# Performance work log

Measured on AMD Instinct MI355X. Metric: run time of the kernel, lower is better.

## Reference

```python
import jax, jax.numpy as jnp
import numpy as np

B, N, ENC = 64, 49, 2048
DEC, ATT, EMB, V, TP1 = 512, 512, 300, 10000, 31


def setup_inputs() -> dict:
    key = jax.random.key(0)
    ks = jax.random.split(key, 20)
    s = 0.02
    inp = {
        "features": jax.random.normal(ks[0], (B, N, ENC), jnp.float32),
        "captions": jax.random.randint(ks[1], (B, TP1), 0, V, jnp.int64),
        "emb": jax.random.normal(ks[2], (V, EMB), jnp.float32) * s,
        "U_w": jax.random.normal(ks[3], (ATT, ENC), jnp.float32) * s,
        "U_b": jnp.zeros((ATT,), jnp.float32),
        "W_w": jax.random.normal(ks[4], (ATT, DEC), jnp.float32) * s,
        "W_b": jnp.zeros((ATT,), jnp.float32),
        "A_w": jax.random.normal(ks[5], (1, ATT), jnp.float32) * s,
        "A_b": jnp.zeros((1,), jnp.float32),
        "initH_w": jax.random.normal(ks[6], (DEC, ENC), jnp.float32) * s,
        "initH_b": jnp.zeros((DEC,), jnp.float32),
        "initC_w": jax.random.normal(ks[7], (DEC, ENC), jnp.float32) * s,
        "initC_b": jnp.zeros((DEC,), jnp.float32),
        "ih_w": jax.random.normal(ks[8], (4 * DEC, EMB + ENC), jnp.float32) * s,
        "ih_b": jnp.zeros((4 * DEC,), jnp.float32),
        "hh_w": jax.random.normal(ks[9], (4 * DEC, DEC), jnp.float32) * s,
        "hh_b": jnp.zeros((4 * DEC,), jnp.float32),
        "fcn_w": jax.random.normal(ks[10], (V, DEC), jnp.float32) * s,
        "fcn_b": jnp.zeros((V,), jnp.float32),
    }
    return inp


def reference(features, captions, emb, U_w, U_b, W_w, W_b, A_w, A_b,
              initH_w, initH_b, initC_w, initC_b,
              ih_w, ih_b, hh_w, hh_b, fcn_w, fcn_b):
    # embeds: [B, T+1, EMB]  (prembed lookup, frozen table)
    embeds = emb[captions]
    T = captions.shape[1] - 1  # static

    # init_hidden_state
    mean_f = features.mean(axis=1)                  # [B, ENC]
    h0 = mean_f @ initH_w.T + initH_b               # [B, DEC]
    c0 = mean_f @ initC_w.T + initC_b

    # U(features) is step-invariant: hoist out of the loop (same math)
    u_hs = jnp.einsum('bne,ae->bna', features, U_w) + U_b  # [B, N, ATT]

    xs = jnp.swapaxes(embeds[:, :T], 0, 1)          # [T, B, EMB]

    def step(carry, x):
        h, c = carry
        # additive attention
        w_ah = h @ W_w.T + W_b                       # [B, ATT]
        comb = jnp.tanh(u_hs + w_ah[:, None, :])     # [B, N, ATT]
        scores = jnp.einsum('bna,a->bn', comb, A_w[0]) + A_b[0]
        alpha = jax.nn.softmax(scores, axis=1)       # [B, N]
        context = jnp.einsum('bn,bne->be', alpha, features)  # [B, ENC]
        # LSTMCell
        lstm_in = jnp.concatenate([x, context], axis=1)
        gates = lstm_in @ ih_w.T + ih_b + h @ hh_w.T + hh_b
        i, f, g, o = jnp.split(gates, 4, axis=1)
        i, f, o = jax.nn.sigmoid(i), jax.nn.sigmoid(f), jax.nn.sigmoid(o)
        g = jnp.tanh(g)
        c = f * c + i * g
        h = o * jnp.tanh(c)
        # dropout in eval mode = identity
        out = h @ fcn_w.T + fcn_b                    # [B, V]
        return (h, c), (out, alpha)

    _, (preds, alphas) = jax.lax.scan(step, (h0, c0), xs)
    preds = jnp.swapaxes(preds, 0, 1)                # [B, T, V]
    alphas = jnp.swapaxes(alphas, 0, 1)              # [B, T, N]
    return preds, alphas
```

## Files before the change

### kernel.cpp

```cpp
#include <hip/hip_runtime.h>
#include <math.h>

#define B 64
#define NN 49
#define ENC 2048
#define DEC 512
#define ATT 512
#define EMB 300
#define VOC 10000
#define TT 30

typedef __attribute__((ext_vector_type(4))) float f32x4;
typedef __attribute__((ext_vector_type(4))) short s16x4;
typedef __attribute__((ext_vector_type(8))) short s16x8;
typedef unsigned short u16;

__device__ __forceinline__ float fast_tanh(float x) {
    float e = __expf(2.f * x);
    return 1.f - 2.f / (e + 1.f);
}
__device__ __forceinline__ float sigmoidf(float x) {
    return 1.f / (1.f + __expf(-x));
}
__device__ __forceinline__ u16 f2bf(float x) {
    unsigned u = __float_as_uint(x);
    unsigned r = u + 0x7FFFu + ((u >> 16) & 1u);
    return (u16)(r >> 16);
}
__device__ __forceinline__ float bf2f(u16 u) {
    return __uint_as_float((unsigned)u << 16);
}
__device__ __forceinline__ void split_bf16(float x, short& hi, short& lo) {
    u16 h = f2bf(x);
    float hf = __uint_as_float((unsigned)h << 16);
    hi = (short)h;
    lo = (short)f2bf(x - hf);
}
__device__ __forceinline__ s16x8 ld8(const short* p) {
    s16x4 a = *(const s16x4*)p;
    s16x4 b = *(const s16x4*)(p + 4);
    return __builtin_shufflevector(a, b, 0, 1, 2, 3, 4, 5, 6, 7);
}

__global__ __launch_bounds__(512) void mfma_nt(
    const float* __restrict__ A, int lda,
    const float* __restrict__ Bm, int ldb,
    const float* __restrict__ bias,
    float* __restrict__ C, int ldc,
    int M, int N, int K, int mode)
{
    __shared__ short Ah[128][40];
    __shared__ short Al[128][40];
    __shared__ short Bh[128][40];
    __shared__ short Bl[128][40];

    const int tid = threadIdx.x;
    const int m0 = blockIdx.y * 128, n0 = blockIdx.x * 128;
    const int wid = tid >> 6, lane = tid & 63;
    const int wm = wid >> 2, wn = wid & 3;
    const int lrow = lane & 15;
    const int lko = (lane >> 4) * 8;
    const int srow = tid >> 2;
    const int sk = (tid & 3) * 8;

    f32x4 acc[4][2];
    #pragma unroll
    for (int i = 0; i < 4; ++i)
        #pragma unroll
        for (int j = 0; j < 2; ++j)
            acc[i][j] = (f32x4){0.f, 0.f, 0.f, 0.f};

    const int nkt = (K + 31) >> 5;
    for (int kt = 0; kt < nkt; ++kt) {
        const int kb0 = kt * 32 + sk;
        {
            const int gr = m0 + srow;
            float v[8];
            if (gr < M && kb0 + 7 < K) {
                const float* p = A + (size_t)gr * lda + kb0;
                float4 x0 = *(const float4*)p;
                float4 x1 = *(const float4*)(p + 4);
                v[0] = x0.x; v[1] = x0.y; v[2] = x0.z; v[3] = x0.w;
                v[4] = x1.x; v[5] = x1.y; v[6] = x1.z; v[7] = x1.w;
            } else {
                #pragma unroll
                for (int j = 0; j < 8; ++j)
                    v[j] = (gr < M && kb0 + j < K) ? A[(size_t)gr * lda + kb0 + j] : 0.f;
            }
            s16x4 h0, h1, l0, l1;
            #pragma unroll
            for (int j = 0; j < 4; ++j) { short h, l; split_bf16(v[j], h, l); h0[j] = h; l0[j] = l; }
            #pragma unroll
            for (int j = 0; j < 4; ++j) { short h, l; split_bf16(v[4 + j], h, l); h1[j] = h; l1[j] = l; }
            *(s16x4*)&Ah[srow][sk] = h0; *(s16x4*)&Ah[srow][sk + 4] = h1;
            *(s16x4*)&Al[srow][sk] = l0; *(s16x4*)&Al[srow][sk + 4] = l1;
        }
        {
            const int gc = n0 + srow;
            float v[8];
            if (gc < N && kb0 + 7 < K) {
                const float* p = Bm + (size_t)gc * ldb + kb0;
                float4 x0 = *(const float4*)p;
                float4 x1 = *(const float4*)(p + 4);
                v[0] = x0.x; v[1] = x0.y; v[2] = x0.z; v[3] = x0.w;
                v[4] = x1.x; v[5] = x1.y; v[6] = x1.z; v[7] = x1.w;
            } else {
                #pragma unroll
                for (int j = 0; j < 8; ++j)
                    v[j] = (gc < N && kb0 + j < K) ? Bm[(size_t)gc * ldb + kb0 + j] : 0.f;
            }
            s16x4 h0, h1, l0, l1;
            #pragma unroll
            for (int j = 0; j < 4; ++j) { short h, l; split_bf16(v[j], h, l); h0[j] = h; l0[j] = l; }
            #pragma unroll
            for (int j = 0; j < 4; ++j) { short h, l; split_bf16(v[4 + j], h, l); h1[j] = h; l1[j] = l; }
            *(s16x4*)&Bh[srow][sk] = h0; *(s16x4*)&Bh[srow][sk + 4] = h1;
            *(s16x4*)&Bl[srow][sk] = l0; *(s16x4*)&Bl[srow][sk + 4] = l1;
        }
        __syncthreads();

        s16x8 bh[2], bl[2];
        #pragma unroll
        for (int nr = 0; nr < 2; ++nr) {
            const int col = wn * 32 + nr * 16 + lrow;
            bh[nr] = ld8(&Bh[col][lko]);
            bl[nr] = ld8(&Bl[col][lko]);
        }
        #pragma unroll
        for (int mr = 0; mr < 4; ++mr) {
            const int row = wm * 64 + mr * 16 + lrow;
            s16x8 ah = ld8(&Ah[row][lko]);
            s16x8 al = ld8(&Al[row][lko]);
            #pragma unroll
            for (int nr = 0; nr < 2; ++nr) {
                acc[mr][nr] = __builtin_amdgcn_mfma_f32_16x16x32_bf16(ah, bh[nr], acc[mr][nr], 0, 0, 0);
                acc[mr][nr] = __builtin_amdgcn_mfma_f32_16x16x32_bf16(ah, bl[nr], acc[mr][nr], 0, 0, 0);
                acc[mr][nr] = __builtin_amdgcn_mfma_f32_16x16x32_bf16(al, bh[nr], acc[mr][nr], 0, 0, 0);
            }
        }
        __syncthreads();
    }

    #pragma unroll
    for (int mr = 0; mr < 4; ++mr) {
        #pragma unroll
        for (int nr = 0; nr < 2; ++nr) {
            #pragma unroll
            for (int r = 0; r < 4; ++r) {
                const int row = m0 + wm * 64 + mr * 16 + (lane >> 4) * 4 + r;
                const int col = n0 + wn * 32 + nr * 16 + (lane & 15);
                if (row < M && col < N)
                    C[(size_t)row * ldc + col] = acc[mr][nr][r] + (bias ? bias[col] : 0.f);
            }
        }
    }
}

__global__ __launch_bounds__(512) void mfma_cat(
    const u16* __restrict__ fhi, const u16* __restrict__ flo,
    const float* __restrict__ U_w, const float* __restrict__ U_b,
    const float* __restrict__ ih_w,
    u16* __restrict__ uhs16, u16* __restrict__ fW16, int M)
{
    __shared__ short Ah[128][40];
    __shared__ short Al[128][40];
    __shared__ short Bh[128][40];
    __shared__ short Bl[128][40];

    const int tid = threadIdx.x;
    const int m0 = blockIdx.y * 128, n0 = blockIdx.x * 128;
    const int wid = tid >> 6, lane = tid & 63;
    const int wm = wid >> 2, wn = wid & 3;
    const int lrow = lane & 15;
    const int lko = (lane >> 4) * 8;
    const int srow = tid >> 2;
    const int sk = (tid & 3) * 8;

    const int gc = n0 + srow;
    const float* bp = (gc < 512) ? (U_w + (size_t)gc * 2048)
                                 : (ih_w + (size_t)(gc - 512) * 2348 + 300);
    const int gr = m0 + srow;
    const u16* ahp = fhi + (size_t)gr * 2048;
    const u16* alp = flo + (size_t)gr * 2048;

    f32x4 acc[4][2];
    #pragma unroll
    for (int i = 0; i < 4; ++i)
        #pragma unroll
        for (int j = 0; j < 2; ++j)
            acc[i][j] = (f32x4){0.f, 0.f, 0.f, 0.f};

    for (int kt = 0; kt < 64; ++kt) {
        const int kb0 = kt * 32 + sk;
        {
            s16x8 vh = {0,0,0,0,0,0,0,0}, vl = {0,0,0,0,0,0,0,0};
            if (gr < M) {
                vh = *(const s16x8*)(ahp + kb0);
                vl = *(const s16x8*)(alp + kb0);
            }
            *(s16x8*)&Ah[srow][sk] = vh;
            *(s16x8*)&Al[srow][sk] = vl;
        }
        {
            float4 x0 = *(const float4*)(bp + kb0);
            float4 x1 = *(const float4*)(bp + kb0 + 4);
            float v[8] = {x0.x, x0.y, x0.z, x0.w, x1.x, x1.y, x1.z, x1.w};
            s16x4 h0, h1, l0, l1;
            #pragma unroll
            for (int j = 0; j < 4; ++j) { short h, l; split_bf16(v[j], h, l); h0[j] = h; l0[j] = l; }
            #pragma unroll
            for (int j = 0; j < 4; ++j) { short h, l; split_bf16(v[4 + j], h, l); h1[j] = h; l1[j] = l; }
            *(s16x4*)&Bh[srow][sk] = h0; *(s16x4*)&Bh[srow][sk + 4] = h1;
            *(s16x4*)&Bl[srow][sk] = l0; *(s16x4*)&Bl[srow][sk + 4] = l1;
        }
        __syncthreads();

        s16x8 bh[2], bl[2];
        #pragma unroll
        for (int nr = 0; nr < 2; ++nr) {
            const int col = wn * 32 + nr * 16 + lrow;
            bh[nr] = ld8(&Bh[col][lko]);
            bl[nr] = ld8(&Bl[col][lko]);
        }
        #pragma unroll
        for (int mr = 0; mr < 4; ++mr) {
            const int row = wm * 64 + mr * 16 + lrow;
            s16x8 ah = ld8(&Ah[row][lko]);
            s16x8 al = ld8(&Al[row][lko]);
            #pragma unroll
            for (int nr = 0; nr < 2; ++nr) {
                acc[mr][nr] = __builtin_amdgcn_mfma_f32_16x16x32_bf16(ah, bh[nr], acc[mr][nr], 0, 0, 0);
                acc[mr][nr] = __builtin_amdgcn_mfma_f32_16x16x32_bf16(ah, bl[nr], acc[mr][nr], 0, 0, 0);
                acc[mr][nr] = __builtin_amdgcn_mfma_f32_16x16x32_bf16(al, bh[nr], acc[mr][nr], 0, 0, 0);
            }
        }
        __syncthreads();
    }

    #pragma unroll
    for (int mr = 0; mr < 4; ++mr) {
        #pragma unroll
        for (int nr = 0; nr < 2; ++nr) {
            #pragma unroll
            for (int r = 0; r < 4; ++r) {
                const int row = m0 + wm * 64 + mr * 16 + (lane >> 4) * 4 + r;
                const int col = n0 + wn * 32 + nr * 16 + (lane & 15);
                if (row < M) {
                    if (col < 512)
                        uhs16[(size_t)row * 512 + col] = f2bf(acc[mr][nr][r] + U_b[col]);
                    else
                        fW16[(size_t)row * 2048 + (col - 512)] = f2bf(acc[mr][nr][r]);
                }
            }
        }
    }
}

__global__ __launch_bounds__(512) void mfma_pre(
    const u16* __restrict__ Ahg, const u16* __restrict__ Alg,
    const u16* __restrict__ Bhg, const u16* __restrict__ Blg,
    const float* __restrict__ bias,
    float* __restrict__ C, int M, int N)
{
    __shared__ short Ah[128][40];
    __shared__ short Al[128][40];
    __shared__ short Bh[128][40];
    __shared__ short Bl[128][40];

    const int tid = threadIdx.x;
    const int m0 = blockIdx.y * 128, n0 = blockIdx.x * 128;
    const int wid = tid >> 6, lane = tid & 63;
    const int wm = wid >> 2, wn = wid & 3;
    const int lrow = lane & 15;
    const int lko = (lane >> 4) * 8;
    const int srow = tid >> 2;
    const int sk = (tid & 3) * 8;

    f32x4 acc[4][2];
    #pragma unroll
    for (int i = 0; i < 4; ++i)
        #pragma unroll
        for (int j = 0; j < 2; ++j)
            acc[i][j] = (f32x4){0.f, 0.f, 0.f, 0.f};

    for (int kt = 0; kt < 16; ++kt) {
        const int kb0 = kt * 32 + sk;
        {
            const int gr = m0 + srow;
            s16x8 vh = {0,0,0,0,0,0,0,0}, vl = {0,0,0,0,0,0,0,0};
            if (gr < M) {
                vh = *(const s16x8*)(Ahg + (size_t)gr * 512 + kb0);
                vl = *(const s16x8*)(Alg + (size_t)gr * 512 + kb0);
            }
            *(s16x8*)&Ah[srow][sk] = vh;
            *(s16x8*)&Al[srow][sk] = vl;
        }
        {
            const int gc = n0 + srow;
            s16x8 vh = {0,0,0,0,0,0,0,0}, vl = {0,0,0,0,0,0,0,0};
            if (gc < N) {
                vh = *(const s16x8*)(Bhg + (size_t)gc * 512 + kb0);
                vl = *(const s16x8*)(Blg + (size_t)gc * 512 + kb0);
            }
            *(s16x8*)&Bh[srow][sk] = vh;
            *(s16x8*)&Bl[srow][sk] = vl;
        }
        __syncthreads();

        s16x8 bh[2], bl[2];
        #pragma unroll
        for (int nr = 0; nr < 2; ++nr) {
            const int col = wn * 32 + nr * 16 + lrow;
            bh[nr] = ld8(&Bh[col][lko]);
            bl[nr] = ld8(&Bl[col][lko]);
        }
        #pragma unroll
        for (int mr = 0; mr < 4; ++mr) {
            const int row = wm * 64 + mr * 16 + lrow;
            s16x8 ah = ld8(&Ah[row][lko]);
            s16x8 al = ld8(&Al[row][lko]);
            #pragma unroll
            for (int nr = 0; nr < 2; ++nr) {
                acc[mr][nr] = __builtin_amdgcn_mfma_f32_16x16x32_bf16(ah, bh[nr], acc[mr][nr], 0, 0, 0);
                acc[mr][nr] = __builtin_amdgcn_mfma_f32_16x16x32_bf16(ah, bl[nr], acc[mr][nr], 0, 0, 0);
                acc[mr][nr] = __builtin_amdgcn_mfma_f32_16x16x32_bf16(al, bh[nr], acc[mr][nr], 0, 0, 0);
            }
        }
        __syncthreads();
    }

    #pragma unroll
    for (int mr = 0; mr < 4; ++mr) {
        #pragma unroll
        for (int nr = 0; nr < 2; ++nr) {
            #pragma unroll
            for (int r = 0; r < 4; ++r) {
                const int row = m0 + wm * 64 + mr * 16 + (lane >> 4) * 4 + r;
                const int col = n0 + wn * 32 + nr * 16 + (lane & 15);
                if (row < M && col < N) {
                    const float val = acc[mr][nr][r] + bias[col];
                    const int t = row >> 6, bb = row & 63;
                    C[(size_t)bb * (TT * VOC) + (size_t)t * VOC + col] = val;
                }
            }
        }
    }
}

__global__ __launch_bounds__(256) void k_mean(const float* __restrict__ f,
                                              float* __restrict__ mean_f)
{
    const int b = blockIdx.x;
    for (int e = threadIdx.x; e < ENC; e += 256) {
        float s = 0.f;
        for (int n = 0; n < NN; ++n) s += f[(size_t)(b * NN + n) * ENC + e];
        mean_f[(size_t)b * ENC + e] = s * (1.f / 49.f);
    }
}

__global__ __launch_bounds__(256) void k_init_partial(
    const float* __restrict__ mean_f,
    const float* __restrict__ iH_w, const float* __restrict__ iC_w,
    float* __restrict__ pbuf)
{
    const int tid = threadIdx.x;
    const int tx = tid & 15, ty = tid >> 4;
    const int n0 = blockIdx.x * 64;
    const int ks = blockIdx.y;
    __shared__ float As[16][64];
    __shared__ float Bs[16][64];
    float acc[4][4] = {};
    const int lrow = tid >> 2;
    const int lk = (tid & 3) * 4;
    for (int c = 0; c < 8; ++c) {
        const int kk = ks * 128 + c * 16 + lk;
        float4 av = *(const float4*)(mean_f + (size_t)lrow * 2048 + kk);
        const int col = n0 + lrow;
        const float* wp = (col < 512) ? (iH_w + (size_t)col * 2048)
                                      : (iC_w + (size_t)(col - 512) * 2048);
        float4 bv = *(const float4*)(wp + kk);
        As[lk + 0][lrow] = av.x; As[lk + 1][lrow] = av.y;
        As[lk + 2][lrow] = av.z; As[lk + 3][lrow] = av.w;
        Bs[lk + 0][lrow] = bv.x; Bs[lk + 1][lrow] = bv.y;
        Bs[lk + 2][lrow] = bv.z; Bs[lk + 3][lrow] = bv.w;
        __syncthreads();
        #pragma unroll
        for (int k = 0; k < 16; ++k) {
            float4 a = *(const float4*)&As[k][ty * 4];
            float4 b = *(const float4*)&Bs[k][tx * 4];
            acc[0][0] += a.x * b.x; acc[0][1] += a.x * b.y; acc[0][2] += a.x * b.z; acc[0][3] += a.x * b.w;
            acc[1][0] += a.y * b.x; acc[1][1] += a.y * b.y; acc[1][2] += a.y * b.z; acc[1][3] += a.y * b.w;
            acc[2][0] += a.z * b.x; acc[2][1] += a.z * b.y; acc[2][2] += a.z * b.z; acc[2][3] += a.z * b.w;
            acc[3][0] += a.w * b.x; acc[3][1] += a.w * b.y; acc[3][2] += a.w * b.z; acc[3][3] += a.w * b.w;
        }
        __syncthreads();
    }
    #pragma unroll
    for (int i = 0; i < 4; ++i) {
        const int r = ty * 4 + i;
        #pragma unroll
        for (int j = 0; j < 4; ++j)
            pbuf[(size_t)(ks * 64 + r) * 1024 + n0 + tx * 4 + j] = acc[i][j];
    }
}

__global__ __launch_bounds__(256) void k_init_reduce(
    const float* __restrict__ pbuf,
    const float* __restrict__ iH_b, const float* __restrict__ iC_b,
    float* __restrict__ h_cur, float* __restrict__ c_cur)
{
    const int idx = blockIdx.x * 256 + threadIdx.x;
    const int r = idx >> 10, c = idx & 1023;
    float s = 0.f;
    #pragma unroll
    for (int ks = 0; ks < 16; ++ks) s += pbuf[(size_t)(ks * 64 + r) * 1024 + c];
    if (c < 512) h_cur[r * 512 + c] = s + iH_b[c];
    else         c_cur[r * 512 + (c - 512)] = s + iC_b[c - 512];
}

__global__ __launch_bounds__(256) void k_embed(const int* __restrict__ cap,
                                               const float* __restrict__ emb,
                                               float* __restrict__ embeds)
{
    const int r = blockIdx.x;
    const int t = r >> 6, b = r & 63;
    const int c = cap[b * 31 + t];
    for (int j = threadIdx.x; j < EMB; j += 256)
        embeds[(size_t)r * EMB + j] = emb[(size_t)c * EMB + j];
}

__global__ void k_bias2(const float* __restrict__ a, const float* __restrict__ b,
                        float* __restrict__ o)
{
    const int j = blockIdx.x * 256 + threadIdx.x;
    if (j < 2048) o[j] = a[j] + b[j];
}

__global__ __launch_bounds__(256) void k_split(const float* __restrict__ src,
                                               u16* __restrict__ hi, u16* __restrict__ lo,
                                               int n)
{
    const int i = (blockIdx.x * 256 + threadIdx.x) * 4;
    if (i >= n) return;
    f32x4 v = *(const f32x4*)(src + i);
    s16x4 h4, l4;
    #pragma unroll
    for (int j = 0; j < 4; ++j) { short h, l; split_bf16(v[j], h, l); h4[j] = h; l4[j] = l; }
    *(s16x4*)(hi + i) = h4;
    *(s16x4*)(lo + i) = l4;
}

__global__ __launch_bounds__(256) void k_hw4(
    const float* __restrict__ h,
    const float* __restrict__ W_w, const float* __restrict__ W_b,
    const float* __restrict__ hh_w,
    float* __restrict__ wahp, float* __restrict__ ghhp)
{
    const int tid = threadIdx.x;
    const int tx = tid & 15, ty = tid >> 4;
    const int n0 = blockIdx.x * 64;
    const int ks = blockIdx.y;
    const float* Bp; const float* biasp; float* Cp; int c0, ldc;
    if (n0 < 512) { Bp = W_w + (size_t)n0 * 512; biasp = (ks == 0) ? W_b : nullptr; Cp = wahp + (size_t)ks * 32768; c0 = n0; ldc = 512; }
    else { Bp = hh_w + (size_t)(n0 - 512) * 512; biasp = nullptr; Cp = ghhp + (size_t)ks * 131072; c0 = n0 - 512; ldc = 2048; }

    __shared__ float As[64][68];
    __shared__ float Bs[64][68];
    float acc[4][4] = {};
    const int rt = tid >> 2;
    const int cs = (tid & 3) * 16;

    for (int kh = 0; kh < 2; ++kh) {
        const int kbase = ks * 128 + kh * 64;
        #pragma unroll
        for (int i = 0; i < 4; ++i) {
            const int c = cs + i * 4;
            *(f32x4*)&As[rt][c] = *(const f32x4*)(h + (size_t)rt * 512 + kbase + c);
            *(f32x4*)&Bs[rt][c] = *(const f32x4*)(Bp + (size_t)rt * 512 + kbase + c);
        }
        __syncthreads();
        #pragma unroll
        for (int k4 = 0; k4 < 16; ++k4) {
            f32x4 a0 = *(const f32x4*)&As[ty * 4 + 0][k4 * 4];
            f32x4 a1 = *(const f32x4*)&As[ty * 4 + 1][k4 * 4];
            f32x4 a2 = *(const f32x4*)&As[ty * 4 + 2][k4 * 4];
            f32x4 a3 = *(const f32x4*)&As[ty * 4 + 3][k4 * 4];
            f32x4 b0 = *(const f32x4*)&Bs[tx * 4 + 0][k4 * 4];
            f32x4 b1 = *(const f32x4*)&Bs[tx * 4 + 1][k4 * 4];
            f32x4 b2 = *(const f32x4*)&Bs[tx * 4 + 2][k4 * 4];
            f32x4 b3 = *(const f32x4*)&Bs[tx * 4 + 3][k4 * 4];
            #pragma unroll
            for (int e = 0; e < 4; ++e) {
                acc[0][0] += a0[e] * b0[e]; acc[0][1] += a0[e] * b1[e];
                acc[0][2] += a0[e] * b2[e]; acc[0][3] += a0[e] * b3[e];
                acc[1][0] += a1[e] * b0[e]; acc[1][1] += a1[e] * b1[e];
                acc[1][2] += a1[e] * b2[e]; acc[1][3] += a1[e] * b3[e];
                acc[2][0] += a2[e] * b0[e]; acc[2][1] += a2[e] * b1[e];
                acc[2][2] += a2[e] * b2[e]; acc[2][3] += a2[e] * b3[e];
                acc[3][0] += a3[e] * b0[e]; acc[3][1] += a3[e] * b1[e];
                acc[3][2] += a3[e] * b2[e]; acc[3][3] += a3[e] * b3[e];
            }
        }
        __syncthreads();
    }
    #pragma unroll
    for (int i = 0; i < 4; ++i) {
        const int r = ty * 4 + i;
        #pragma unroll
        for (int j = 0; j < 4; ++j) {
            const int cc = c0 + tx * 4 + j;
            Cp[(size_t)r * ldc + cc] = acc[i][j] + (biasp ? biasp[cc] : 0.f);
        }
    }
}

__global__ __launch_bounds__(512) void k_fused4(
    const u16* __restrict__ uhs16,
    const float* __restrict__ A_w, const float* __restrict__ A_b,
    const float* __restrict__ wahp,
    const float* __restrict__ ghhp,
    const float* __restrict__ pre_x,
    const u16* __restrict__ fW16,
    float* __restrict__ h_cur, float* __restrict__ c_cur,
    u16* __restrict__ Hall_h, u16* __restrict__ Hall_l,
    float* __restrict__ alphas, int s)
{
    const int bb = blockIdx.x;
    const int qq = blockIdx.y;
    const int tid = threadIdx.x;
    const int lane = tid & 63, w = tid >> 6;
    __shared__ float wah_l[512];
    __shared__ float red[64];
    __shared__ float al[64];
    __shared__ float ghl[512];
    __shared__ float gl[512];

    const int gate = tid >> 7, dloc = tid & 127;
    const int jcol = gate * 512 + qq * 128 + dloc;
    float ghv = pre_x[(size_t)(s * 64 + bb) * 2048 + jcol]
              + ghhp[(size_t)bb * 2048 + jcol]
              + ghhp[131072 + (size_t)bb * 2048 + jcol]
              + ghhp[262144 + (size_t)bb * 2048 + jcol]
              + ghhp[393216 + (size_t)bb * 2048 + jcol];
    float wv = wahp[bb * 512 + tid] + wahp[32768 + bb * 512 + tid]
             + wahp[65536 + bb * 512 + tid] + wahp[98304 + bb * 512 + tid];
    const float cload = c_cur[bb * 512 + qq * 128 + (tid & 127)];

    const int a0 = lane * 8;
    float aw8[8];
    #pragma unroll
    for (int k = 0; k < 8; ++k) aw8[k] = A_w[a0 + k];

    const int ngf = tid & 7, r = tid >> 3;
    const int gf = r >> 4, oc = r & 15;
    const int jb = gf * 512 + qq * 128 + oc * 8;
    const u16* fb = fW16 + (size_t)bb * NN * 2048 + jb;
    s16x8 pf[7];
    #pragma unroll
    for (int i = 0; i < 7; ++i) {
        const int n = ngf + 8 * i;
        if (n < NN) pf[i] = *(const s16x8*)(fb + (size_t)n * 2048);
        else        pf[i] = (s16x8){0, 0, 0, 0, 0, 0, 0, 0};
    }

    ghl[tid] = ghv;
    wah_l[tid] = wv;
    __syncthreads();

    float wh8[8];
    #pragma unroll
    for (int k = 0; k < 8; ++k) wh8[k] = wah_l[a0 + k];

    const u16* ub = uhs16 + (size_t)(bb * NN) * 512 + a0;
    #pragma unroll
    for (int i = 0; i < 7; ++i) {
        const int n = w + 8 * i;
        const int nc = (n < NN) ? n : 0;
        const s16x8 uv = *(const s16x8*)(ub + (size_t)nc * 512);
        float acc = 0.f;
        #pragma unroll
        for (int k = 0; k < 8; ++k)
            acc += aw8[k] * fast_tanh(bf2f((u16)uv[k]) + wh8[k]);
        #pragma unroll
        for (int m = 32; m; m >>= 1) acc += __shfl_xor(acc, m, 64);
        if (lane == 0 && n < NN) red[n] = acc + A_b[0];
    }
    __syncthreads();

    if (tid < 64) {
        const float sc = (tid < NN) ? red[tid] : -1e30f;
        float mx = sc;
        #pragma unroll
        for (int m = 32; m; m >>= 1) mx = fmaxf(mx, __shfl_xor(mx, m, 64));
        float e = (tid < NN) ? __expf(sc - mx) : 0.f;
        float sum = e;
        #pragma unroll
        for (int m = 32; m; m >>= 1) sum += __shfl_xor(sum, m, 64);
        const float av = e / sum;
        al[tid] = av;
        if (qq == 0 && tid < NN)
            alphas[(size_t)bb * (TT * NN) + (size_t)s * NN + tid] = av;
    }
    __syncthreads();

    float a8[8] = {0.f, 0.f, 0.f, 0.f, 0.f, 0.f, 0.f, 0.f};
    #pragma unroll
    for (int i = 0; i < 7; ++i) {
        const int n = ngf + 8 * i;
        const float av = al[n];
        #pragma unroll
        for (int k = 0; k < 8; ++k)
            a8[k] += av * bf2f((u16)pf[i][k]);
    }
    #pragma unroll
    for (int m = 1; m < 8; m <<= 1)
        #pragma unroll
        for (int k = 0; k < 8; ++k)
            a8[k] += __shfl_xor(a8[k], m, 64);
    if (ngf == 0) {
        const int base = gf * 128 + oc * 8;
        #pragma unroll
        for (int k = 0; k < 8; ++k)
            gl[base + k] = a8[k] + ghl[base + k];
    }
    __syncthreads();

    if (tid < 128) {
        const int dd = qq * 128 + tid;
        const float ig = sigmoidf(gl[tid]);
        const float fg = sigmoidf(gl[128 + tid]);
        const float gg = fast_tanh(gl[256 + tid]);
        const float og = sigmoidf(gl[384 + tid]);
        const float cv = fg * cload + ig * gg;
        const float hv = og * fast_tanh(cv);
        c_cur[bb * 512 + dd] = cv;
        h_cur[bb * 512 + dd] = hv;
        short hh, hl;
        split_bf16(hv, hh, hl);
        Hall_h[(size_t)(s * 64 + bb) * 512 + dd] = (u16)hh;
        Hall_l[(size_t)(s * 64 + bb) * 512 + dd] = (u16)hl;
    }
}

extern "C" void kernel_launch(void* const* d_in, const int* in_sizes, int n_in,
                              void* d_out, int out_size, void* d_ws, size_t ws_size,
                              hipStream_t stream)
{
    const float* features = (const float*)d_in[0];
    const int*   captions = (const int*)d_in[1];
    const float* emb      = (const float*)d_in[2];
    const float* U_w      = (const float*)d_in[3];
    const float* U_b      = (const float*)d_in[4];
    const float* W_w      = (const float*)d_in[5];
    const float* W_b      = (const float*)d_in[6];
    const float* A_w      = (const float*)d_in[7];
    const float* A_b      = (const float*)d_in[8];
    const float* iH_w     = (const float*)d_in[9];
    const float* iH_b     = (const float*)d_in[10];
    const float* iC_w     = (const float*)d_in[11];
    const float* iC_b     = (const float*)d_in[12];
    const float* ih_w     = (const float*)d_in[13];
    const float* ih_b     = (const float*)d_in[14];
    const float* hh_w     = (const float*)d_in[15];
    const float* hh_b     = (const float*)d_in[16];
    const float* fcn_w    = (const float*)d_in[17];
    const float* fcn_b    = (const float*)d_in[18];

    float* out    = (float*)d_out;
    float* alphas = out + (size_t)B * TT * VOC;

    float* ws     = (float*)d_ws;
    u16*  fW16    = (u16*)ws;
    u16*  uhs16   = (u16*)(ws + 3211264);
    float* pre_x  = ws + 4014080;
    u16*  Hall_h  = (u16*)(ws + 7946240);
    u16*  Hall_l  = (u16*)(ws + 8437760);
    float* mean_f = ws + 8929280;
    float* h_cur  = ws + 9060352;
    float* c_cur  = ws + 9093120;
    float* wahp   = ws + 9125888;
    float* ghhp   = ws + 9256960;
    float* embeds = ws + 9781248;
    float* bias2  = ws + 10357248;
    u16*  fhi     = (u16*)(ws + 10359296);
    u16*  flo     = (u16*)(ws + 13570560);
    float* pbuf   = ws;
    u16*  fcnw_h  = fhi;
    u16*  fcnw_l  = flo;

    k_mean<<<64, 256, 0, stream>>>(features, mean_f);
    k_init_partial<<<dim3(16, 16), 256, 0, stream>>>(mean_f, iH_w, iC_w, pbuf);
    k_init_reduce<<<256, 256, 0, stream>>>(pbuf, iH_b, iC_b, h_cur, c_cur);

    k_embed<<<1920, 256, 0, stream>>>(captions, emb, embeds);
    k_bias2<<<8, 256, 0, stream>>>(ih_b, hh_b, bias2);
    k_split<<<6272, 256, 0, stream>>>(features, fhi, flo, B * NN * ENC);
    mfma_cat<<<dim3(20, 25), 512, 0, stream>>>(fhi, flo, U_w, U_b, ih_w, uhs16, fW16, B * NN);
    mfma_nt<<<dim3(16, 15), 512, 0, stream>>>(embeds, EMB, ih_w, 2348, bias2, pre_x, 2048, TT * B, 2048, EMB, 0);

    k_hw4<<<dim3(40, 4), 256, 0, stream>>>(h_cur, W_w, W_b, hh_w, wahp, ghhp);
    for (int s = 0; s < TT; ++s) {
        k_fused4<<<dim3(64, 4), 512, 0, stream>>>(uhs16, A_w, A_b, wahp, ghhp, pre_x, fW16,
                                                  h_cur, c_cur, Hall_h, Hall_l, alphas, s);
        if (s < TT - 1)
            k_hw4<<<dim3(40, 4), 256, 0, stream>>>(h_cur, W_w, W_b, hh_w, wahp, ghhp);
    }

    k_split<<<5000, 256, 0, stream>>>(fcn_w, fcnw_h, fcnw_l, VOC * DEC);
    mfma_pre<<<dim3(79, 15), 512, 0, stream>>>(Hall_h, Hall_l, fcnw_h, fcnw_l, fcn_b,
                                               out, TT * B, VOC);
}
```

Before: 925.1 us.

## Pre-split ih_w, fuse embedding gather into GEMM, widen recurrent split-K

Result: no change. 928.6 us (+0.4%).

```diff
diff --git a/kernel.cpp b/kernel.cpp
--- a/kernel.cpp
+++ b/kernel.cpp
@@ -42,12 +42,11 @@
     return __builtin_shufflevector(a, b, 0, 1, 2, 3, 4, 5, 6, 7);
 }
 
-__global__ __launch_bounds__(512) void mfma_nt(
-    const float* __restrict__ A, int lda,
-    const float* __restrict__ Bm, int ldb,
-    const float* __restrict__ bias,
-    float* __restrict__ C, int ldc,
-    int M, int N, int K, int mode)
+__global__ __launch_bounds__(512) void mfma_cat2(
+    const u16* __restrict__ fhi, const u16* __restrict__ flo,
+    const float* __restrict__ U_w, const float* __restrict__ U_b,
+    const u16* __restrict__ ihw_h, const u16* __restrict__ ihw_l,
+    u16* __restrict__ uhs16, u16* __restrict__ fW16, int M)
 {
     __shared__ short Ah[128][40];
     __shared__ short Al[128][40];
@@ -63,122 +62,7 @@
     const int srow = tid >> 2;
     const int sk = (tid & 3) * 8;
 
-    f32x4 acc[4][2];
-    #pragma unroll
-    for (int i = 0; i < 4; ++i)
-        #pragma unroll
-        for (int j = 0; j < 2; ++j)
-            acc[i][j] = (f32x4){0.f, 0.f, 0.f, 0.f};
-
-    const int nkt = (K + 31) >> 5;
-    for (int kt = 0; kt < nkt; ++kt) {
-        const int kb0 = kt * 32 + sk;
-        {
-            const int gr = m0 + srow;
-            float v[8];
-            if (gr < M && kb0 + 7 < K) {
-                const float* p = A + (size_t)gr * lda + kb0;
-                float4 x0 = *(const float4*)p;
-                float4 x1 = *(const float4*)(p + 4);
-                v[0] = x0.x; v[1] = x0.y; v[2] = x0.z; v[3] = x0.w;
-                v[4] = x1.x; v[5] = x1.y; v[6] = x1.z; v[7] = x1.w;
-            } else {
-                #pragma unroll
-                for (int j = 0; j < 8; ++j)
-                    v[j] = (gr < M && kb0 + j < K) ? A[(size_t)gr * lda + kb0 + j] : 0.f;
-            }
-            s16x4 h0, h1, l0, l1;
-            #pragma unroll
-            for (int j = 0; j < 4; ++j) { short h, l; split_bf16(v[j], h, l); h0[j] = h; l0[j] = l; }
-            #pragma unroll
-            for (int j = 0; j < 4; ++j) { short h, l; split_bf16(v[4 + j], h, l); h1[j] = h; l1[j] = l; }
-            *(s16x4*)&Ah[srow][sk] = h0; *(s16x4*)&Ah[srow][sk + 4] = h1;
-            *(s16x4*)&Al[srow][sk] = l0; *(s16x4*)&Al[srow][sk + 4] = l1;
-        }
-        {
-            const int gc = n0 + srow;
-            float v[8];
-            if (gc < N && kb0 + 7 < K) {
-                const float* p = Bm + (size_t)gc * ldb + kb0;
-                float4 x0 = *(const float4*)p;
-                float4 x1 = *(const float4*)(p + 4);
-                v[0] = x0.x; v[1] = x0.y; v[2] = x0.z; v[3] = x0.w;
-                v[4] = x1.x; v[5] = x1.y; v[6] = x1.z; v[7] = x1.w;
-            } else {
-                #pragma unroll
-                for (int j = 0; j < 8; ++j)
-                    v[j] = (gc < N && kb0 + j < K) ? Bm[(size_t)gc * ldb + kb0 + j] : 0.f;
-            }
-            s16x4 h0, h1, l0, l1;
-            #pragma unroll
-            for (int j = 0; j < 4; ++j) { short h, l; split_bf16(v[j], h, l); h0[j] = h; l0[j] = l; }
-            #pragma unroll
-            for (int j = 0; j < 4; ++j) { short h, l; split_bf16(v[4 + j], h, l); h1[j] = h; l1[j] = l; }
-            *(s16x4*)&Bh[srow][sk] = h0; *(s16x4*)&Bh[srow][sk + 4] = h1;
-            *(s16x4*)&Bl[srow][sk] = l0; *(s16x4*)&Bl[srow][sk + 4] = l1;
-        }
-        __syncthreads();
-
-        s16x8 bh[2], bl[2];
-        #pragma unroll
-        for (int nr = 0; nr < 2; ++nr) {
-            const int col = wn * 32 + nr * 16 + lrow;
-            bh[nr] = ld8(&Bh[col][lko]);
-            bl[nr] = ld8(&Bl[col][lko]);
-        }
-        #pragma unroll
-        for (int mr = 0; mr < 4; ++mr) {
-            const int row = wm * 64 + mr * 16 + lrow;
-            s16x8 ah = ld8(&Ah[row][lko]);
-            s16x8 al = ld8(&Al[row][lko]);
-            #pragma unroll
-            for (int nr = 0; nr < 2; ++nr) {
-                acc[mr][nr] = __builtin_amdgcn_mfma_f32_16x16x32_bf16(ah, bh[nr], acc[mr][nr], 0, 0, 0);
-                acc[mr][nr] = __builtin_amdgcn_mfma_f32_16x16x32_bf16(ah, bl[nr], acc[mr][nr], 0, 0, 0);
-                acc[mr][nr] = __builtin_amdgcn_mfma_f32_16x16x32_bf16(al, bh[nr], acc[mr][nr], 0, 0, 0);
-            }
-        }
-        __syncthreads();
-    }
-
-    #pragma unroll
-    for (int mr = 0; mr < 4; ++mr) {
-        #pragma unroll
-        for (int nr = 0; nr < 2; ++nr) {
-            #pragma unroll
-            for (int r = 0; r < 4; ++r) {
-                const int row = m0 + wm * 64 + mr * 16 + (lane >> 4) * 4 + r;
-                const int col = n0 + wn * 32 + nr * 16 + (lane & 15);
-                if (row < M && col < N)
-                    C[(size_t)row * ldc + col] = acc[mr][nr][r] + (bias ? bias[col] : 0.f);
-            }
-        }
-    }
-}
-
-__global__ __launch_bounds__(512) void mfma_cat(
-    const u16* __restrict__ fhi, const u16* __restrict__ flo,
-    const float* __restrict__ U_w, const float* __restrict__ U_b,
-    const float* __restrict__ ih_w,
-    u16* __restrict__ uhs16, u16* __restrict__ fW16, int M)
-{
-    __shared__ short Ah[128][40];
-    __shared__ short Al[128][40];
-    __shared__ short Bh[128][40];
-    __shared__ short Bl[128][40];
-
-    const int tid = threadIdx.x;
-    const int m0 = blockIdx.y * 128, n0 = blockIdx.x * 128;
-    const int wid = tid >> 6, lane = tid & 63;
-    const int wm = wid >> 2, wn = wid & 3;
-    const int lrow = lane & 15;
-    const int lko = (lane >> 4) * 8;
-    const int srow = tid >> 2;
-    const int sk = (tid & 3) * 8;
-
     const int gc = n0 + srow;
-    const float* bp = (gc < 512) ? (U_w + (size_t)gc * 2048)
-                                 : (ih_w + (size_t)(gc - 512) * 2348 + 300);
     const int gr = m0 + srow;
     const u16* ahp = fhi + (size_t)gr * 2048;
     const u16* alp = flo + (size_t)gr * 2048;
@@ -201,7 +85,8 @@
             *(s16x8*)&Ah[srow][sk] = vh;
             *(s16x8*)&Al[srow][sk] = vl;
         }
-        {
+        if (n0 < 512) {
+            const float* bp = U_w + (size_t)gc * 2048;
             float4 x0 = *(const float4*)(bp + kb0);
             float4 x1 = *(const float4*)(bp + kb0 + 4);
             float v[8] = {x0.x, x0.y, x0.z, x0.w, x1.x, x1.y, x1.z, x1.w};
@@ -212,6 +97,9 @@
             for (int j = 0; j < 4; ++j) { short h, l; split_bf16(v[4 + j], h, l); h1[j] = h; l1[j] = l; }
             *(s16x4*)&Bh[srow][sk] = h0; *(s16x4*)&Bh[srow][sk + 4] = h1;
             *(s16x4*)&Bl[srow][sk] = l0; *(s16x4*)&Bl[srow][sk + 4] = l1;
+        } else {
+            *(s16x8*)&Bh[srow][sk] = *(const s16x8*)(ihw_h + (size_t)(gc - 512) * 2048 + kb0);
+            *(s16x8*)&Bl[srow][sk] = *(const s16x8*)(ihw_l + (size_t)(gc - 512) * 2048 + kb0);
         }
         __syncthreads();
 
@@ -251,6 +139,120 @@
                     else
                         fW16[(size_t)row * 2048 + (col - 512)] = f2bf(acc[mr][nr][r]);
                 }
+            }
+        }
+    }
+}
+
+__global__ __launch_bounds__(512) void mfma_prex(
+    const int* __restrict__ cap,
+    const float* __restrict__ emb,
+    const float* __restrict__ ih_w,
+    const float* __restrict__ bias2,
+    float* __restrict__ pre_x)
+{
+    __shared__ short Ah[128][40];
+    __shared__ short Al[128][40];
+    __shared__ short Bh[128][40];
+    __shared__ short Bl[128][40];
+
+    const int tid = threadIdx.x;
+    const int m0 = blockIdx.y * 128, n0 = blockIdx.x * 128;
+    const int wid = tid >> 6, lane = tid & 63;
+    const int wm = wid >> 2, wn = wid & 3;
+    const int lrow = lane & 15;
+    const int lko = (lane >> 4) * 8;
+    const int srow = tid >> 2;
+    const int sk = (tid & 3) * 8;
+
+    const int gr = m0 + srow;
+    const int tt = gr >> 6, bbs = gr & 63;
+    const float* ap = emb + (size_t)cap[bbs * 31 + tt] * 300;
+    const int gc = n0 + srow;
+    const float* bp = ih_w + (size_t)gc * 2348;
+
+    f32x4 acc[4][2];
+    #pragma unroll
+    for (int i = 0; i < 4; ++i)
+        #pragma unroll
+        for (int j = 0; j < 2; ++j)
+            acc[i][j] = (f32x4){0.f, 0.f, 0.f, 0.f};
+
+    for (int kt = 0; kt < 10; ++kt) {
+        const int kb0 = kt * 32 + sk;
+        {
+            float v[8];
+            if (kb0 + 7 < 300) {
+                float4 x0 = *(const float4*)(ap + kb0);
+                float4 x1 = *(const float4*)(ap + kb0 + 4);
+                v[0] = x0.x; v[1] = x0.y; v[2] = x0.z; v[3] = x0.w;
+                v[4] = x1.x; v[5] = x1.y; v[6] = x1.z; v[7] = x1.w;
+            } else {
+                #pragma unroll
+                for (int j = 0; j < 8; ++j)
+                    v[j] = (kb0 + j < 300) ? ap[kb0 + j] : 0.f;
+            }
+            s16x4 h0, h1, l0, l1;
+            #pragma unroll
+            for (int j = 0; j < 4; ++j) { short h, l; split_bf16(v[j], h, l); h0[j] = h; l0[j] = l; }
+            #pragma unroll
+            for (int j = 0; j < 4; ++j) { short h, l; split_bf16(v[4 + j], h, l); h1[j] = h; l1[j] = l; }
+            *(s16x4*)&Ah[srow][sk] = h0; *(s16x4*)&Ah[srow][sk + 4] = h1;
+            *(s16x4*)&Al[srow][sk] = l0; *(s16x4*)&Al[srow][sk + 4] = l1;
+        }
+        {
+            float v[8];
+            if (kb0 + 7 < 300) {
+                float4 x0 = *(const float4*)(bp + kb0);
+                float4 x1 = *(const float4*)(bp + kb0 + 4);
+                v[0] = x0.x; v[1] = x0.y; v[2] = x0.z; v[3] = x0.w;
+                v[4] = x1.x; v[5] = x1.y; v[6] = x1.z; v[7] = x1.w;
+            } else {
+                #pragma unroll
+                for (int j = 0; j < 8; ++j)
+                    v[j] = (kb0 + j < 300) ? bp[kb0 + j] : 0.f;
+            }
+            s16x4 h0, h1, l0, l1;
+            #pragma unroll
+            for (int j = 0; j < 4; ++j) { short h, l; split_bf16(v[j], h, l); h0[j] = h; l0[j] = l; }
+            #pragma unroll
+            for (int j = 0; j < 4; ++j) { short h, l; split_bf16(v[4 + j], h, l); h1[j] = h; l1[j] = l; }
+            *(s16x4*)&Bh[srow][sk] = h0; *(s16x4*)&Bh[srow][sk + 4] = h1;
+            *(s16x4*)&Bl[srow][sk] = l0; *(s16x4*)&Bl[srow][sk + 4] = l1;
+        }
+        __syncthreads();
+
+        s16x8 bh[2], bl[2];
+        #pragma unroll
+        for (int nr = 0; nr < 2; ++nr) {
+            const int col = wn * 32 + nr * 16 + lrow;
+            bh[nr] = ld8(&Bh[col][lko]);
+            bl[nr] = ld8(&Bl[col][lko]);
+        }
+        #pragma unroll
+        for (int mr = 0; mr < 4; ++mr) {
+            const int row = wm * 64 + mr * 16 + lrow;
+            s16x8 ah = ld8(&Ah[row][lko]);
+            s16x8 al = ld8(&Al[row][lko]);
+            #pragma unroll
+            for (int nr = 0; nr < 2; ++nr) {
+                acc[mr][nr] = __builtin_amdgcn_mfma_f32_16x16x32_bf16(ah, bh[nr], acc[mr][nr], 0, 0, 0);
+                acc[mr][nr] = __builtin_amdgcn_mfma_f32_16x16x32_bf16(ah, bl[nr], acc[mr][nr], 0, 0, 0);
+                acc[mr][nr] = __builtin_amdgcn_mfma_f32_16x16x32_bf16(al, bh[nr], acc[mr][nr], 0, 0, 0);
+            }
+        }
+        __syncthreads();
+    }
+
+    #pragma unroll
+    for (int mr = 0; mr < 4; ++mr) {
+        #pragma unroll
+        for (int nr = 0; nr < 2; ++nr) {
+            #pragma unroll
+            for (int r = 0; r < 4; ++r) {
+                const int row = m0 + wm * 64 + mr * 16 + (lane >> 4) * 4 + r;
+                const int col = n0 + wn * 32 + nr * 16 + (lane & 15);
+                pre_x[(size_t)row * 2048 + col] = acc[mr][nr][r] + bias2[col];
             }
         }
     }
@@ -418,17 +420,6 @@
     else         c_cur[r * 512 + (c - 512)] = s + iC_b[c - 512];
 }
 
-__global__ __launch_bounds__(256) void k_embed(const int* __restrict__ cap,
-                                               const float* __restrict__ emb,
-                                               float* __restrict__ embeds)
-{
-    const int r = blockIdx.x;
-    const int t = r >> 6, b = r & 63;
-    const int c = cap[b * 31 + t];
-    for (int j = threadIdx.x; j < EMB; j += 256)
-        embeds[(size_t)r * EMB + j] = emb[(size_t)c * EMB + j];
-}
-
 __global__ void k_bias2(const float* __restrict__ a, const float* __restrict__ b,
                         float* __restrict__ o)
 {
@@ -450,7 +441,26 @@
     *(s16x4*)(lo + i) = l4;
 }
 
-__global__ __launch_bounds__(256) void k_hw4(
+__global__ __launch_bounds__(256) void k_splitW(const float* __restrict__ ih_w,
+                                                u16* __restrict__ hi, u16* __restrict__ lo)
+{
+    const int r = blockIdx.x;
+    const float* src = ih_w + (size_t)r * 2348 + 300;
+    u16* hp = hi + (size_t)r * 2048;
+    u16* lp = lo + (size_t)r * 2048;
+    const int c = threadIdx.x * 8;
+    #pragma unroll
+    for (int g = 0; g < 2; ++g) {
+        f32x4 v = *(const f32x4*)(src + c + g * 4);
+        s16x4 h4, l4;
+        #pragma unroll
+        for (int j = 0; j < 4; ++j) { short h, l; split_bf16(v[j], h, l); h4[j] = h; l4[j] = l; }
+        *(s16x4*)(hp + c + g * 4) = h4;
+        *(s16x4*)(lp + c + g * 4) = l4;
+    }
+}
+
+__global__ __launch_bounds__(256) void k_hw8(
     const float* __restrict__ h,
     const float* __restrict__ W_w, const float* __restrict__ W_b,
     const float* __restrict__ hh_w,
@@ -469,52 +479,49 @@
     float acc[4][4] = {};
     const int rt = tid >> 2;
     const int cs = (tid & 3) * 16;
-
-    for (int kh = 0; kh < 2; ++kh) {
-        const int kbase = ks * 128 + kh * 64;
-        #pragma unroll
-        for (int i = 0; i < 4; ++i) {
-            const int c = cs + i * 4;
-            *(f32x4*)&As[rt][c] = *(const f32x4*)(h + (size_t)rt * 512 + kbase + c);
-            *(f32x4*)&Bs[rt][c] = *(const f32x4*)(Bp + (size_t)rt * 512 + kbase + c);
-        }
-        __syncthreads();
-        #pragma unroll
-        for (int k4 = 0; k4 < 16; ++k4) {
-            f32x4 a0 = *(const f32x4*)&As[ty * 4 + 0][k4 * 4];
-            f32x4 a1 = *(const f32x4*)&As[ty * 4 + 1][k4 * 4];
-            f32x4 a2 = *(const f32x4*)&As[ty * 4 + 2][k4 * 4];
-            f32x4 a3 = *(const f32x4*)&As[ty * 4 + 3][k4 * 4];
-            f32x4 b0 = *(const f32x4*)&Bs[tx * 4 + 0][k4 * 4];
-            f32x4 b1 = *(const f32x4*)&Bs[tx * 4 + 1][k4 * 4];
-            f32x4 b2 = *(const f32x4*)&Bs[tx * 4 + 2][k4 * 4];
-            f32x4 b3 = *(const f32x4*)&Bs[tx * 4 + 3][k4 * 4];
-            #pragma unroll
-            for (int e = 0; e < 4; ++e) {
-                acc[0][0] += a0[e] * b0[e]; acc[0][1] += a0[e] * b1[e];
-                acc[0][2] += a0[e] * b2[e]; acc[0][3] += a0[e] * b3[e];
-                acc[1][0] += a1[e] * b0[e]; acc[1][1] += a1[e] * b1[e];
-                acc[1][2] += a1[e] * b2[e]; acc[1][3] += a1[e] * b3[e];
-                acc[2][0] += a2[e] * b0[e]; acc[2][1] += a2[e] * b1[e];
-                acc[2][2] += a2[e] * b2[e]; acc[2][3] += a2[e] * b3[e];
-                acc[3][0] += a3[e] * b0[e]; acc[3][1] += a3[e] * b1[e];
-                acc[3][2] += a3[e] * b2[e]; acc[3][3] += a3[e] * b3[e];
-            }
-        }
-        __syncthreads();
-    }
+    const int kbase = ks * 64;
+
     #pragma unroll
     for (int i = 0; i < 4; ++i) {
-        const int r = ty * 4 + i;
+        const int c = cs + i * 4;
+        *(f32x4*)&As[rt][c] = *(const f32x4*)(h + (size_t)rt * 512 + kbase + c);
+        *(f32x4*)&Bs[rt][c] = *(const f32x4*)(Bp + (size_t)rt * 512 + kbase + c);
+    }
+    __syncthreads();
+    #pragma unroll 4
+    for (int k4 = 0; k4 < 16; ++k4) {
+        f32x4 a0 = *(const f32x4*)&As[ty + 0][k4 * 4];
+        f32x4 a1 = *(const f32x4*)&As[ty + 16][k4 * 4];
+        f32x4 a2 = *(const f32x4*)&As[ty + 32][k4 * 4];
+        f32x4 a3 = *(const f32x4*)&As[ty + 48][k4 * 4];
+        f32x4 b0 = *(const f32x4*)&Bs[tx + 0][k4 * 4];
+        f32x4 b1 = *(const f32x4*)&Bs[tx + 16][k4 * 4];
+        f32x4 b2 = *(const f32x4*)&Bs[tx + 32][k4 * 4];
+        f32x4 b3 = *(const f32x4*)&Bs[tx + 48][k4 * 4];
+        #pragma unroll
+        for (int e = 0; e < 4; ++e) {
+            acc[0][0] += a0[e] * b0[e]; acc[0][1] += a0[e] * b1[e];
+            acc[0][2] += a0[e] * b2[e]; acc[0][3] += a0[e] * b3[e];
+            acc[1][0] += a1[e] * b0[e]; acc[1][1] += a1[e] * b1[e];
+            acc[1][2] += a1[e] * b2[e]; acc[1][3] += a1[e] * b3[e];
+            acc[2][0] += a2[e] * b0[e]; acc[2][1] += a2[e] * b1[e];
+            acc[2][2] += a2[e] * b2[e]; acc[2][3] += a2[e] * b3[e];
+            acc[3][0] += a3[e] * b0[e]; acc[3][1] += a3[e] * b1[e];
+            acc[3][2] += a3[e] * b2[e]; acc[3][3] += a3[e] * b3[e];
+        }
+    }
+    #pragma unroll
+    for (int i = 0; i < 4; ++i) {
+        const int r = ty + i * 16;
         #pragma unroll
         for (int j = 0; j < 4; ++j) {
-            const int cc = c0 + tx * 4 + j;
+            const int cc = c0 + tx + j * 16;
             Cp[(size_t)r * ldc + cc] = acc[i][j] + (biasp ? biasp[cc] : 0.f);
         }
     }
 }
 
-__global__ __launch_bounds__(512) void k_fused4(
+__global__ __launch_bounds__(512) void k_fused5(
     const u16* __restrict__ uhs16,
     const float* __restrict__ A_w, const float* __restrict__ A_b,
     const float* __restrict__ wahp,
@@ -537,13 +544,14 @@
 
     const int gate = tid >> 7, dloc = tid & 127;
     const int jcol = gate * 512 + qq * 128 + dloc;
-    float ghv = pre_x[(size_t)(s * 64 + bb) * 2048 + jcol]
-              + ghhp[(size_t)bb * 2048 + jcol]
-              + ghhp[131072 + (size_t)bb * 2048 + jcol]
-              + ghhp[262144 + (size_t)bb * 2048 + jcol]
-              + ghhp[393216 + (size_t)bb * 2048 + jcol];
-    float wv = wahp[bb * 512 + tid] + wahp[32768 + bb * 512 + tid]
-             + wahp[65536 + bb * 512 + tid] + wahp[98304 + bb * 512 + tid];
+    float ghv = pre_x[(size_t)(s * 64 + bb) * 2048 + jcol];
+    #pragma unroll
+    for (int i = 0; i < 8; ++i)
+        ghv += ghhp[(size_t)i * 131072 + (size_t)bb * 2048 + jcol];
+    float wv = 0.f;
+    #pragma unroll
+    for (int i = 0; i < 8; ++i)
+        wv += wahp[(size_t)i * 32768 + bb * 512 + tid];
     const float cload = c_cur[bb * 512 + qq * 128 + (tid & 127)];
 
     const int a0 = lane * 8;
@@ -675,16 +683,17 @@
     float* pre_x  = ws + 4014080;
     u16*  Hall_h  = (u16*)(ws + 7946240);
     u16*  Hall_l  = (u16*)(ws + 8437760);
-    float* mean_f = ws + 8929280;
-    float* h_cur  = ws + 9060352;
-    float* c_cur  = ws + 9093120;
-    float* wahp   = ws + 9125888;
+    float* h_cur  = ws + 8929280;
+    float* c_cur  = ws + 8962048;
+    float* wahp   = ws + 8994816;
     float* ghhp   = ws + 9256960;
-    float* embeds = ws + 9781248;
-    float* bias2  = ws + 10357248;
-    u16*  fhi     = (u16*)(ws + 10359296);
-    u16*  flo     = (u16*)(ws + 13570560);
+    float* bias2  = ws + 10305536;
+    u16*  fhi     = (u16*)(ws + 10307584);
+    u16*  flo     = (u16*)(ws + 13518848);
     float* pbuf   = ws;
+    float* mean_f = ws + 1048576;
+    u16*  ihw_h   = (u16*)pre_x;
+    u16*  ihw_l   = (u16*)(ws + 6111232);
     u16*  fcnw_h  = fhi;
     u16*  fcnw_l  = flo;
 
@@ -692,21 +701,22 @@
     k_init_partial<<<dim3(16, 16), 256, 0, stream>>>(mean_f, iH_w, iC_w, pbuf);
     k_init_reduce<<<256, 256, 0, stream>>>(pbuf, iH_b, iC_b, h_cur, c_cur);
 
-    k_embed<<<1920, 256, 0, stream>>>(captions, emb, embeds);
     k_bias2<<<8, 256, 0, stream>>>(ih_b, hh_b, bias2);
     k_split<<<6272, 256, 0, stream>>>(features, fhi, flo, B * NN * ENC);
-    mfma_cat<<<dim3(20, 25), 512, 0, stream>>>(fhi, flo, U_w, U_b, ih_w, uhs16, fW16, B * NN);
-    mfma_nt<<<dim3(16, 15), 512, 0, stream>>>(embeds, EMB, ih_w, 2348, bias2, pre_x, 2048, TT * B, 2048, EMB, 0);
-
-    k_hw4<<<dim3(40, 4), 256, 0, stream>>>(h_cur, W_w, W_b, hh_w, wahp, ghhp);
+    k_splitW<<<2048, 256, 0, stream>>>(ih_w, ihw_h, ihw_l);
+    mfma_cat2<<<dim3(20, 25), 512, 0, stream>>>(fhi, flo, U_w, U_b, ihw_h, ihw_l,
+                                                uhs16, fW16, B * NN);
+    k_split<<<5000, 256, 0, stream>>>(fcn_w, fcnw_h, fcnw_l, VOC * DEC);
+    mfma_prex<<<dim3(16, 15), 512, 0, stream>>>(captions, emb, ih_w, bias2, pre_x);
+
+    k_hw8<<<dim3(40, 8), 256, 0, stream>>>(h_cur, W_w, W_b, hh_w, wahp, ghhp);
     for (int s = 0; s < TT; ++s) {
-        k_fused4<<<dim3(64, 4), 512, 0, stream>>>(uhs16, A_w, A_b, wahp, ghhp, pre_x, fW16,
+        k_fused5<<<dim3(64, 4), 512, 0, stream>>>(uhs16, A_w, A_b, wahp, ghhp, pre_x, fW16,
                                                   h_cur, c_cur, Hall_h, Hall_l, alphas, s);
         if (s < TT - 1)
-            k_hw4<<<dim3(40, 4), 256, 0, stream>>>(h_cur, W_w, W_b, hh_w, wahp, ghhp);
-    }
-
-    k_split<<<5000, 256, 0, stream>>>(fcn_w, fcnw_h, fcnw_l, VOC * DEC);
+            k_hw8<<<dim3(40, 8), 256, 0, stream>>>(h_cur, W_w, W_b, hh_w, wahp, ghhp);
+    }
+
     mfma_pre<<<dim3(79, 15), 512, 0, stream>>>(Hall_h, Hall_l, fcnw_h, fcnw_l, fcn_b,
                                                out, TT * B, VOC);
 }
```
